# Optimization experiments

Hardware: AMD Instinct MI355X
Metric: run time of the kernel (lower is better)

Reference implementation:

```python
import jax, jax.numpy as jnp
import numpy as np
import math

B, S = 4, 1024
V, D, L, H, F, MAXLEN = 32000, 1024, 6, 16, 4096, 2048
DH = D // H
NUM_BUCKETS, MAX_DIST = 32, 256
REL_SCALE = 64.0 ** 0.5
EPS = 1e-5


def setup_inputs() -> dict:
    key = jax.random.key(0)
    ks = iter(jax.random.split(key, 32))
    sd = 0.02
    inp = {
        'src': jax.random.randint(next(ks), (B, S), 0, V),
        'src_mask': jnp.ones((B, 1, 1, S), dtype=jnp.int32),
        'tok_emb': jax.random.normal(next(ks), (V, D), jnp.float32) * sd,
        'pos_emb': jax.random.normal(next(ks), (MAXLEN, D), jnp.float32) * sd,
        'Wq': jax.random.normal(next(ks), (L, D, D), jnp.float32) * sd,
        'bq': jnp.zeros((L, D), jnp.float32),
        'Wk': jax.random.normal(next(ks), (L, D, D), jnp.float32) * sd,
        'bk': jnp.zeros((L, D), jnp.float32),
        'Wv': jax.random.normal(next(ks), (L, D, D), jnp.float32) * sd,
        'bv': jnp.zeros((L, D), jnp.float32),
        'Wo': jax.random.normal(next(ks), (L, D, D), jnp.float32) * sd,
        'bo': jnp.zeros((L, D), jnp.float32),
        'rel_bias': jax.random.normal(next(ks), (L, NUM_BUCKETS, H), jnp.float32) * sd,
        'ln1_g': jnp.ones((L, D), jnp.float32),
        'ln1_b': jnp.zeros((L, D), jnp.float32),
        'W1': jax.random.normal(next(ks), (L, D, F), jnp.float32) * sd,
        'b1': jnp.zeros((L, F), jnp.float32),
        'W2': jax.random.normal(next(ks), (L, F, D), jnp.float32) * sd,
        'b2': jnp.zeros((L, D), jnp.float32),
        'ln2_g': jnp.ones((L, D), jnp.float32),
        'ln2_b': jnp.zeros((L, D), jnp.float32),
    }
    return inp


def _rel_pos_bucket(seq_len):
    # non-causal bucketing (T5-style), matching the torch source
    q = jnp.arange(seq_len)
    k = jnp.arange(seq_len)
    n = q[:, None] - k[None, :]          # == -(k - q)
    nb = NUM_BUCKETS // 2                # 16
    ret = (n < 0).astype(jnp.int32) * nb
    n = jnp.abs(n)
    max_exact = nb // 2                  # 8
    is_small = n < max_exact
    val_large = max_exact + (
        jnp.log(jnp.maximum(n, 1).astype(jnp.float32) / max_exact)
        / math.log(MAX_DIST / max_exact) * (nb - max_exact)
    ).astype(jnp.int32)
    val_large = jnp.minimum(val_large, nb - 1)
    return ret + jnp.where(is_small, n, val_large)  # [S,S] in [0,32)


def _layer_norm(x, g, b):
    mu = jnp.mean(x, axis=-1, keepdims=True)
    var = jnp.var(x, axis=-1, keepdims=True)
    return (x - mu) * jax.lax.rsqrt(var + EPS) * g + b


def reference(src, src_mask, tok_emb, pos_emb, Wq, bq, Wk, bk, Wv, bv, Wo, bo,
              rel_bias, ln1_g, ln1_b, W1, b1, W2, b2, ln2_g, ln2_b):
    seq_len = src.shape[1]
    bucket = _rel_pos_bucket(seq_len)                      # [S,S] int
    x = tok_emb[src] * jnp.sqrt(jnp.float32(D)) + pos_emb[jnp.arange(seq_len)][None]
    scale = jnp.sqrt(jnp.float32(DH))
    neg = jnp.float32(-1e10)

    def layer(x, p):
        (wq, bq_, wk, bk_, wv, bv_, wo, bo_, rb, g1, b1_, w1, bb1, w2, bb2, g2, b2_) = p
        Q = (x @ wq + bq_).reshape(B, seq_len, H, DH)
        K = (x @ wk + bk_).reshape(B, seq_len, H, DH)
        Vv = (x @ wv + bv_).reshape(B, seq_len, H, DH)
        energy = jnp.einsum('bqhd,bkhd->bhqk', Q, K) / scale
        energy = jnp.where(src_mask == 0, neg, energy)
        bias = rb[bucket]                                  # [S,S,H]
        energy = energy + jnp.transpose(bias, (2, 0, 1))[None] * REL_SCALE
        attn = jax.nn.softmax(energy, axis=-1)
        o = jnp.einsum('bhqk,bkhd->bqhd', attn, Vv).reshape(B, seq_len, D)
        o = o @ wo + bo_
        x = _layer_norm(x + o, g1, b1_)
        f = jax.nn.relu(x @ w1 + bb1) @ w2 + bb2
        x = _layer_norm(x + f, g2, b2_)
        return x, None

    params = (Wq, bq, Wk, bk, Wv, bv, Wo, bo, rel_bias,
              ln1_g, ln1_b, W1, b1, W2, b2, ln2_g, ln2_b)
    x, _ = jax.lax.scan(layer, x, params)
    return x
```

## Files before the change

### kernel.cpp

```cpp
#include <hip/hip_runtime.h>

#define B_ 4
#define S_ 1024
#define D_ 1024
#define F_ 4096
#define H_ 16
#define L_ 6
#define M_ (B_*S_)

typedef unsigned short u16;
typedef __attribute__((ext_vector_type(4))) unsigned short u16x4;
typedef __attribute__((ext_vector_type(8))) short s16x8;
typedef __attribute__((ext_vector_type(8))) __bf16 bf16x8;
typedef __attribute__((ext_vector_type(4))) float f32x4;

typedef const __attribute__((address_space(1))) unsigned int gu32;
typedef __attribute__((address_space(3))) unsigned int su32;

__device__ __forceinline__ u16 f2bf(float f) {
  union { float f; unsigned u; } v; v.f = f;
  unsigned u = v.u;
  return (u16)((u + 0x7fffu + ((u >> 16) & 1u)) >> 16);
}
__device__ __forceinline__ float bf2f(u16 h) {
  union { unsigned u; float f; } v; v.u = (unsigned)h << 16; return v.f;
}

__device__ __forceinline__ f32x4 mfma16(s16x8 a, s16x8 b, f32x4 c) {
  return __builtin_amdgcn_mfma_f32_16x16x32_bf16(
      __builtin_bit_cast(bf16x8, a), __builtin_bit_cast(bf16x8, b), c, 0, 0, 0);
}

__device__ __forceinline__ void gload16(const void* g, void* s) {
  __builtin_amdgcn_global_load_lds((gu32*)g, (su32*)s, 16, 0, 0);
}

template<int OUTMODE>
__device__ __forceinline__ void gemm128_body(
    const u16* __restrict__ A, const u16* __restrict__ Bt,
    const float* __restrict__ b0, const float* __restrict__ b1,
    const float* __restrict__ b2, u16* __restrict__ Ch,
    int N, int K, int kbeg, int kend)
{
  __shared__ __align__(16) u16 As[128 * 64];
  __shared__ __align__(16) u16 Bs[128 * 64];
  const int tid = threadIdx.x, lane = tid & 63, w = tid >> 6;
  const int bm = blockIdx.x * 128, bn = blockIdx.y * 128;
  const int wm = (w >> 1) * 64, wn = (w & 1) * 64;

  f32x4 acc[4][4];
#pragma unroll
  for (int i = 0; i < 4; i++)
#pragma unroll
    for (int j = 0; j < 4; j++) acc[i][j] = {0.f, 0.f, 0.f, 0.f};

  for (int k0 = kbeg; k0 < kend; k0 += 64) {
    __syncthreads();
#pragma unroll
    for (int i = 0; i < 4; i++) {
      const int flat = i * 4096 + w * 1024 + lane * 16;
      const int row = flat >> 7, ce = (flat & 127) >> 1;
      gload16(A + (size_t)(bm + row) * K + k0 + ce, As + i * 2048 + w * 512);
      gload16(Bt + (size_t)(bn + row) * K + k0 + ce, Bs + i * 2048 + w * 512);
    }
    __syncthreads();
#pragma unroll
    for (int kk = 0; kk < 2; kk++) {
      s16x8 af[4], bf[4];
#pragma unroll
      for (int mf = 0; mf < 4; mf++)
        af[mf] = *(const s16x8*)&As[(wm + mf * 16 + (lane & 15)) * 64 + kk * 32 + (lane >> 4) * 8];
#pragma unroll
      for (int nf = 0; nf < 4; nf++)
        bf[nf] = *(const s16x8*)&Bs[(wn + nf * 16 + (lane & 15)) * 64 + kk * 32 + (lane >> 4) * 8];
#pragma unroll
      for (int mf = 0; mf < 4; mf++)
#pragma unroll
        for (int nf = 0; nf < 4; nf++)
          acc[mf][nf] = mfma16(af[mf], bf[nf], acc[mf][nf]);
    }
  }
#pragma unroll
  for (int nf = 0; nf < 4; nf++) {
    const int col = bn + wn + nf * 16 + (lane & 15);
    float bvv = 0.f, sc = 1.0f;
    int zz = 0, lc = col;
    if (OUTMODE == 3) {
      zz = col >> 10; lc = col & 1023;
      const float* bp = (zz == 0) ? b0 : (zz == 1) ? b1 : b2;
      bvv = bp[lc];
      sc = (zz == 0) ? 0.125f : 1.0f;
    }
#pragma unroll
    for (int mf = 0; mf < 4; mf++) {
#pragma unroll
      for (int j = 0; j < 4; j++) {
        const int row = bm + wm + mf * 16 + ((lane >> 4) << 2) + j;
        const float v = acc[mf][nf][j];
        if (OUTMODE == 1) {
          Ch[(size_t)row * N + col] = f2bf(v);
        } else {
          Ch[(size_t)zz * M_ * D_ + (size_t)row * D_ + lc] = f2bf((v + bvv) * sc);
        }
      }
    }
  }
}

__global__ __launch_bounds__(256, 3) void gemm_qkvf(
    const u16* __restrict__ A, const u16* __restrict__ WT,
    const float* __restrict__ bq, const float* __restrict__ bk,
    const float* __restrict__ bv, u16* __restrict__ Out)
{
  gemm128_body<3>(A, WT, bq, bk, bv, Out, 3 * D_, D_, 0, D_);
}

__global__ __launch_bounds__(256, 3) void gemm_osplit2(
    const u16* __restrict__ A, const u16* __restrict__ WT,
    u16* __restrict__ P)
{
  const int z = blockIdx.z;
  gemm128_body<1>(A, WT, nullptr, nullptr, nullptr,
                  P + (size_t)z * M_ * D_, D_, D_, z * 512, z * 512 + 512);
}

__device__ __forceinline__ s16x8 readfrag(const u16* half, int r, int kk, int hi4) {
  const int c = (kk * 64 + hi4 * 16) ^ ((r & 7) << 4);
  return *(const s16x8*)((const char*)half + r * 128 + c);
}

__device__ __forceinline__ void stage_half(
    const u16* __restrict__ src, int ldk, u16* lds_half, int w, int lane)
{
#pragma unroll
  for (int j = 0; j < 2; j++) {
    const int flat = j * 8192 + w * 1024 + lane * 16;
    const int row = flat >> 7;
    const int kb = (flat & 127) ^ ((row & 7) << 4);
    gload16(src + (size_t)row * ldk + (kb >> 1), lds_half + j * 4096 + w * 512);
  }
}

#define BAR     asm volatile("s_barrier" ::: "memory")
#define PH_PRE  asm volatile("s_barrier" ::: "memory"); __builtin_amdgcn_s_setprio(1)
#define PH_POST __builtin_amdgcn_s_setprio(0); __builtin_amdgcn_sched_barrier(0)
#define VM4     asm volatile("s_waitcnt vmcnt(4)" ::: "memory")
#define VM0     asm volatile("s_waitcnt vmcnt(0)" ::: "memory")

#define READ_B(bufhalf) do { \
  _Pragma("unroll") for (int nf = 0; nf < 4; nf++) \
  _Pragma("unroll") for (int kk = 0; kk < 2; kk++) \
    bfr[nf][kk] = readfrag(bufhalf, rb0 + nf * 16 + lo16, kk, hi4); } while (0)
#define READ_A(bufhalf, Q) do { \
  _Pragma("unroll") for (int m = 0; m < 2; m++) \
  _Pragma("unroll") for (int kk = 0; kk < 2; kk++) \
    af[m][kk] = readfrag(bufhalf, (2 * (Q) + m) * 16 + lo16, kk, hi4); } while (0)
#define DO_MFMA(Q) do { \
  _Pragma("unroll") for (int kk = 0; kk < 2; kk++) \
  _Pragma("unroll") for (int m = 0; m < 2; m++) \
  _Pragma("unroll") for (int nf = 0; nf < 4; nf++) \
    acc[2 * (Q) + m][nf] = mfma16(af[m][kk], bfr[nf][kk], acc[2 * (Q) + m][nf]); } while (0)

template<int OUTMODE>
__device__ __forceinline__ void gemm256_body(
    const u16* __restrict__ A, const u16* __restrict__ Bt,
    const float* __restrict__ bias, u16* __restrict__ Ch,
    int N, int K, int kbeg, int kslice)
{
  __shared__ __align__(16) u16 As[2][2][8192];
  __shared__ __align__(16) u16 Bs[2][2][8192];
  const int tid = threadIdx.x, lane = tid & 63, w = tid >> 6;
  const int wr = w >> 2, wc = w & 3;
  const int lo16 = lane & 15, hi4 = lane >> 4;
  const int bm = blockIdx.x * 256, bn = blockIdx.y * 256;
  const int rb0 = (wc & 1) * 64;

  const u16* Abase = A + (size_t)bm * K + kbeg;
  const u16* Bbase = Bt + (size_t)bn * K + kbeg;
  const size_t h1 = (size_t)128 * K;
  const int NT = kslice >> 6, NI = NT >> 1;

  f32x4 acc[8][4];
#pragma unroll
  for (int i = 0; i < 8; i++)
#pragma unroll
    for (int j = 0; j < 4; j++) acc[i][j] = {0.f, 0.f, 0.f, 0.f};

  stage_half(Abase,           K, As[0][0], w, lane);
  stage_half(Abase + h1,      K, As[0][1], w, lane);
  stage_half(Bbase,           K, Bs[0][0], w, lane);
  stage_half(Bbase + h1,      K, Bs[0][1], w, lane);
  stage_half(Abase + 64,      K, As[1][0], w, lane);
  stage_half(Abase + h1 + 64, K, As[1][1], w, lane);
  stage_half(Bbase + 64,      K, Bs[1][0], w, lane);
  stage_half(Bbase + h1 + 64, K, Bs[1][1], w, lane);
  asm volatile("s_waitcnt vmcnt(8)" ::: "memory");
  BAR;

  const u16* Ae = As[0][wr]; const u16* Ao = As[1][wr];
  const u16* Be = Bs[0][wc >> 1]; const u16* Bo = Bs[1][wc >> 1];
  s16x8 af[2][2], bfr[4][2];

  for (int it = 0; it < NI - 1; ++it) {
    READ_B(Be); READ_A(Ae, 0);
    if (it > 0) {
      stage_half(Abase +      (size_t)(2 * it + 1) * 64, K, As[1][0], w, lane);
      stage_half(Abase + h1 + (size_t)(2 * it + 1) * 64, K, As[1][1], w, lane);
    }
    PH_PRE; DO_MFMA(0); PH_POST; BAR;
    READ_A(Ae, 1);
    stage_half(Bbase +      (size_t)(2 * it + 2) * 64, K, Bs[0][0], w, lane);
    PH_PRE; DO_MFMA(1); PH_POST; BAR;
    READ_A(Ae, 2);
    stage_half(Bbase + h1 + (size_t)(2 * it + 2) * 64, K, Bs[0][1], w, lane);
    PH_PRE; DO_MFMA(2); PH_POST; BAR;
    READ_A(Ae, 3);
    PH_PRE; DO_MFMA(3); PH_POST; VM4; BAR;
    READ_B(Bo); READ_A(Ao, 0);
    stage_half(Abase +      (size_t)(2 * it + 2) * 64, K, As[0][0], w, lane);
    stage_half(Abase + h1 + (size_t)(2 * it + 2) * 64, K, As[0][1], w, lane);
    PH_PRE; DO_MFMA(0); PH_POST; BAR;
    READ_A(Ao, 1);
    stage_half(Bbase +      (size_t)(2 * it + 3) * 64, K, Bs[1][0], w, lane);
    PH_PRE; DO_MFMA(1); PH_POST; BAR;
    READ_A(Ao, 2);
    stage_half(Bbase + h1 + (size_t)(2 * it + 3) * 64, K, Bs[1][1], w, lane);
    PH_PRE; DO_MFMA(2); PH_POST; BAR;
    READ_A(Ao, 3);
    PH_PRE; DO_MFMA(3); PH_POST; VM4; BAR;
  }
  READ_B(Be); READ_A(Ae, 0);
  stage_half(Abase +      (size_t)(NT - 1) * 64, K, As[1][0], w, lane);
  stage_half(Abase + h1 + (size_t)(NT - 1) * 64, K, As[1][1], w, lane);
  PH_PRE; DO_MFMA(0); PH_POST; BAR;
  READ_A(Ae, 1);             PH_PRE; DO_MFMA(1); PH_POST; BAR;
  READ_A(Ae, 2);             PH_PRE; DO_MFMA(2); PH_POST; BAR;
  READ_A(Ae, 3);             PH_PRE; DO_MFMA(3); PH_POST; VM0; BAR;
  READ_B(Bo); READ_A(Ao, 0); PH_PRE; DO_MFMA(0); PH_POST; BAR;
  READ_A(Ao, 1);             PH_PRE; DO_MFMA(1); PH_POST; BAR;
  READ_A(Ao, 2);             PH_PRE; DO_MFMA(2); PH_POST; BAR;
  READ_A(Ao, 3);             PH_PRE; DO_MFMA(3); PH_POST;

  const int row0 = bm + wr * 128, col0 = bn + wc * 64;
#pragma unroll
  for (int nf = 0; nf < 4; nf++) {
    const int col = col0 + nf * 16 + lo16;
    const float bv = (OUTMODE == 2) ? bias[col] : 0.f;
#pragma unroll
    for (int mf = 0; mf < 8; mf++) {
#pragma unroll
      for (int j = 0; j < 4; j++) {
        const int row = row0 + mf * 16 + hi4 * 4 + j;
        float v = acc[mf][nf][j];
        if (OUTMODE == 2) v = fmaxf(v + bv, 0.f);
        Ch[(size_t)row * N + col] = f2bf(v);
      }
    }
  }
}

__global__ __launch_bounds__(512, 2) void gemm_ffn1(
    const u16* __restrict__ A, const u16* __restrict__ WT,
    const float* __restrict__ bias, u16* __restrict__ Out)
{
  gemm256_body<2>(A, WT, bias, Out, F_, D_, 0, D_);
}

__global__ __launch_bounds__(512, 2) void gemm_ffn2sp4(
    const u16* __restrict__ A, const u16* __restrict__ WT,
    u16* __restrict__ P)
{
  const int z = blockIdx.z;
  gemm256_body<4>(A, WT, nullptr, P + (size_t)z * M_ * D_,
                  D_, F_, z * 1024, 1024);
}

__global__ __launch_bounds__(256) void transpose_cvt(
    const float* __restrict__ src, u16* __restrict__ dst, int R, int Cc)
{
  __shared__ float t[32][33];
  const int c0 = blockIdx.x * 32, r0 = blockIdx.y * 32;
  const int tx = threadIdx.x & 31, ty = threadIdx.x >> 5;
#pragma unroll
  for (int i = 0; i < 4; i++)
    t[ty + 8 * i][tx] = src[(size_t)(r0 + ty + 8 * i) * Cc + c0 + tx];
  __syncthreads();
#pragma unroll
  for (int i = 0; i < 4; i++)
    dst[(size_t)(c0 + ty + 8 * i) * R + r0 + tx] = f2bf(t[tx][ty + 8 * i]);
}

__global__ __launch_bounds__(256) void transpose4(
    const float* __restrict__ Wq, const float* __restrict__ Wk,
    const float* __restrict__ Wv, const float* __restrict__ Wo,
    u16* __restrict__ WTqkv, u16* __restrict__ WTo)
{
  __shared__ float t[32][33];
  const int z = blockIdx.z;
  const float* src = (z == 0) ? Wq : (z == 1) ? Wk : (z == 2) ? Wv : Wo;
  u16* dst = (z < 3) ? WTqkv + (size_t)z * D_ * D_ : WTo;
  const int c0 = blockIdx.x * 32, r0 = blockIdx.y * 32;
  const int tx = threadIdx.x & 31, ty = threadIdx.x >> 5;
#pragma unroll
  for (int i = 0; i < 4; i++)
    t[ty + 8 * i][tx] = src[(size_t)(r0 + ty + 8 * i) * D_ + c0 + tx];
  __syncthreads();
#pragma unroll
  for (int i = 0; i < 4; i++)
    dst[(size_t)(c0 + ty + 8 * i) * D_ + r0 + tx] = f2bf(t[tx][ty + 8 * i]);
}

__global__ __launch_bounds__(256) void vt_transpose(
    const u16* __restrict__ Vb, u16* __restrict__ Vt)
{
  __shared__ u16 t[64][66];
  const int s0 = blockIdx.x * 64;
  const int bh = blockIdx.y;
  const int b = bh >> 4, h = bh & 15;
  const int tid = threadIdx.x;
  const int row = tid >> 2;
  const int c0 = (tid & 3) * 16;
  const u16* src = Vb + (size_t)(b * S_ + s0 + row) * D_ + h * 64 + c0;
  *(s16x8*)&t[row][c0] = *(const s16x8*)src;
  *(s16x8*)&t[row][c0 + 8] = *(const s16x8*)(src + 8);
  __syncthreads();
  const int dh = tid >> 2;
  const int sc = (tid & 3) * 16;
  s16x8 a, bv;
#pragma unroll
  for (int u = 0; u < 8; u++) a[u] = (short)t[sc + u][dh];
#pragma unroll
  for (int u = 0; u < 8; u++) bv[u] = (short)t[sc + 8 + u][dh];
  u16* dst = Vt + (size_t)(bh * 64 + dh) * S_ + s0 + sc;
  *(s16x8*)dst = a;
  *(s16x8*)(dst + 8) = bv;
}

__global__ __launch_bounds__(256) void build_lut(
    const float* __restrict__ rb, float* __restrict__ lut_g)
{
  const int h = blockIdx.x, l = blockIdx.y;
  for (int idx = threadIdx.x; idx < 2048; idx += 256) {
    const int rel = idx - 1024;
    const int ret = rel < 0 ? 16 : 0;
    const int n = rel < 0 ? -rel : rel;
    int bu;
    if (n < 8) bu = ret + n;
    else {
      const float t = logf((float)n * 0.125f) * (8.0f / 3.4657359027997265f);
      int vl = 8 + (int)t;
      if (vl > 15) vl = 15;
      bu = ret + vl;
    }
    lut_g[(size_t)(l * H_ + h) * 2048 + idx] = rb[l * 512 + bu * 16 + h] * 8.0f;
  }
}

__global__ __launch_bounds__(256) void mask2neg(
    const int* __restrict__ mask, u16* __restrict__ mf)
{
  const int i = blockIdx.x * 256 + threadIdx.x;
  if (i < B_ * S_) mf[i] = mask[i] ? (u16)0 : f2bf(-1e10f);
}

__device__ __forceinline__ s16x8 lds_swz(const u16* base, int row, int cb) {
  const int addr = row * 128 + (cb ^ ((row & 7) << 4));
  return *(const s16x8*)((const char*)base + addr);
}

#define ATTN_STAGE(t, buf) do { \
  const int kt2 = (t) * 64; \
  const int flat2 = tid * 16; \
  const int row2 = flat2 >> 7; \
  const int ce2 = ((flat2 & 127) ^ ((row2 & 7) << 4)) >> 1; \
  gload16(Kb + (size_t)(bS + kt2 + row2) * D_ + hh + ce2, Ks[buf] + w * 512); \
  gload16(Vt + (size_t)(bh * 64 + row2) * S_ + kt2 + ce2, Vs[buf] + w * 512); \
} while (0)

__global__ __launch_bounds__(512, 2) void attn_kernel(
    const u16* __restrict__ Qb, const u16* __restrict__ Kb,
    const u16* __restrict__ Vt, const u16* __restrict__ mask16,
    const float* __restrict__ lut_g, u16* __restrict__ AO)
{
  __shared__ __align__(16) float lut[2048];
  __shared__ __align__(16) u16 maskf[1024];
  __shared__ __align__(16) u16 Ks[2][64 * 64];
  __shared__ __align__(16) u16 Vs[2][64 * 64];
  __shared__ __align__(16) u16 Ps[8][16 * 68];

  const int tid = threadIdx.x;
  const int lane = tid & 63;
  const int w = tid >> 6;
  const int bh = blockIdx.x;
  const int b = bh >> 4, h = bh & 15;
  const int q0 = blockIdx.y * 128 + w * 16;
  const int bS = b * S_, hh = h * 64;
  const int lo16 = lane & 15, hi4 = lane >> 4;

  const float* lsrc = lut_g + (size_t)h * 2048;
  gload16(lsrc + w * 256 + lane * 4, lut + w * 256);
  if (w < 2)
    gload16(mask16 + bS + w * 512 + lane * 8, maskf + w * 512);

  s16x8 qf[2];
#pragma unroll
  for (int kk = 0; kk < 2; kk++)
    qf[kk] = *(const s16x8*)(Qb + (size_t)(bS + q0 + lo16) * D_ + hh +
                             kk * 32 + hi4 * 8);

  s16x8 onesf;
#pragma unroll
  for (int u = 0; u < 8; u++) onesf[u] = (short)((lo16 == 0) ? 0x3F80 : 0);

  f32x4 oacc[5];
#pragma unroll
  for (int i = 0; i < 5; i++) oacc[i] = {0.f, 0.f, 0.f, 0.f};

  ATTN_STAGE(0, 0);
  asm volatile("s_waitcnt vmcnt(0) lgkmcnt(0)" ::: "memory");
  __builtin_amdgcn_s_barrier();

  for (int t = 0; t < S_ / 64; ++t) {
    const int cur = t & 1;
    const int kt = t * 64;
    if (t < S_ / 64 - 1) ATTN_STAGE(t + 1, cur ^ 1);

    f32x4 sacc[4];
#pragma unroll
    for (int i = 0; i < 4; i++) sacc[i] = {0.f, 0.f, 0.f, 0.f};
#pragma unroll
    for (int kk = 0; kk < 2; kk++) {
      const int cb = kk * 64 + hi4 * 16;
#pragma unroll
      for (int nf = 0; nf < 4; nf++) {
        const s16x8 kb = lds_swz(Ks[cur], nf * 16 + lo16, cb);
        sacc[nf] = mfma16(qf[kk], kb, sacc[nf]);
      }
    }

    float kmf[4];
#pragma unroll
    for (int nf = 0; nf < 4; nf++)
      kmf[nf] = bf2f(maskf[kt + nf * 16 + lo16]);

    const int lidx0 = q0 + hi4 * 4 + 1024 - kt - lo16;
#pragma unroll
    for (int j = 0; j < 4; j++) {
      const int lrow = (hi4 << 2) + j;
#pragma unroll
      for (int nf = 0; nf < 4; nf++) {
        const float s = sacc[nf][j] + kmf[nf] + lut[lidx0 + j - nf * 16];
        Ps[w][lrow * 68 + nf * 16 + lo16] = f2bf(__expf(s));
      }
    }

#pragma unroll
    for (int kk = 0; kk < 2; kk++) {
      const s16x8 pa = *(const s16x8*)&Ps[w][lo16 * 68 + kk * 32 + hi4 * 8];
      const int cb = kk * 64 + hi4 * 16;
#pragma unroll
      for (int df = 0; df < 4; df++) {
        const s16x8 vb = lds_swz(Vs[cur], df * 16 + lo16, cb);
        oacc[df] = mfma16(pa, vb, oacc[df]);
      }
      oacc[4] = mfma16(pa, onesf, oacc[4]);
    }

    asm volatile("s_waitcnt vmcnt(0)" ::: "memory");
    __builtin_amdgcn_s_barrier();
  }

  float inv[4];
#pragma unroll
  for (int j = 0; j < 4; j++) {
    const float l = __shfl(oacc[4][j], lane & 48);
    inv[j] = 1.0f / l;
  }
#pragma unroll
  for (int df = 0; df < 4; df++)
#pragma unroll
    for (int j = 0; j < 4; j++) {
      const int qrow = q0 + (hi4 << 2) + j;
      AO[(size_t)(bS + qrow) * D_ + hh + df * 16 + lo16] =
          f2bf(oacc[df][j] * inv[j]);
    }
}

template<int NP>
__global__ __launch_bounds__(256) void ln_fusedb(
    const u16* __restrict__ Xh, const u16* __restrict__ P,
    const float* __restrict__ bias, const float* __restrict__ g,
    const float* __restrict__ be, u16* __restrict__ Yh, float* __restrict__ Yf)
{
  const int row = blockIdx.x;
  const int tid = threadIdx.x;
  const size_t off = (size_t)row * D_;
  const size_t ps = (size_t)M_ * D_;
  const u16x4 xv = ((const u16x4*)(Xh + off))[tid];
  float v[4];
#pragma unroll
  for (int q = 0; q < 4; q++) v[q] = bf2f(xv[q]);
#pragma unroll
  for (int p = 0; p < NP; p++) {
    const u16x4 pv = ((const u16x4*)(P + p * ps + off))[tid];
#pragma unroll
    for (int q = 0; q < 4; q++) v[q] += bf2f(pv[q]);
  }
  const float4 bb = ((const float4*)bias)[tid];
  v[0] += bb.x; v[1] += bb.y; v[2] += bb.z; v[3] += bb.w;

  float sum = v[0] + v[1] + v[2] + v[3];
  float ss = v[0] * v[0] + v[1] * v[1] + v[2] * v[2] + v[3] * v[3];
#pragma unroll
  for (int o = 1; o < 64; o <<= 1) {
    sum += __shfl_xor(sum, o);
    ss += __shfl_xor(ss, o);
  }
  __shared__ float s1[4], s2[4];
  if ((tid & 63) == 0) { s1[tid >> 6] = sum; s2[tid >> 6] = ss; }
  __syncthreads();
  sum = s1[0] + s1[1] + s1[2] + s1[3];
  ss = s2[0] + s2[1] + s2[2] + s2[3];
  const float mu = sum * (1.f / D_);
  const float var = ss * (1.f / D_) - mu * mu;
  const float rstd = rsqrtf(var + 1e-5f);
  const float4 gv = ((const float4*)g)[tid];
  const float4 bv = ((const float4*)be)[tid];
  float y[4];
  y[0] = (v[0] - mu) * rstd * gv.x + bv.x;
  y[1] = (v[1] - mu) * rstd * gv.y + bv.y;
  y[2] = (v[2] - mu) * rstd * gv.z + bv.z;
  y[3] = (v[3] - mu) * rstd * gv.w + bv.w;
  u16x4 hv;
  hv.x = f2bf(y[0]); hv.y = f2bf(y[1]); hv.z = f2bf(y[2]); hv.w = f2bf(y[3]);
  ((u16x4*)(Yh + off))[tid] = hv;
  if (Yf != nullptr) {
    float4 yf; yf.x = y[0]; yf.y = y[1]; yf.z = y[2]; yf.w = y[3];
    ((float4*)(Yf + off))[tid] = yf;
  }
}

__global__ __launch_bounds__(256) void embed_kernel(
    const int* __restrict__ src, const float* __restrict__ tok,
    const float* __restrict__ pos, u16* __restrict__ Xh)
{
  const int row = blockIdx.x;
  const int s = row & (S_ - 1);
  const int t = src[row];
  const int tid = threadIdx.x;
  const float4 tv = ((const float4*)(tok + (size_t)t * D_))[tid];
  const float4 pv = ((const float4*)(pos + (size_t)s * D_))[tid];
  u16x4 hv;
  hv.x = f2bf(tv.x * 32.f + pv.x);
  hv.y = f2bf(tv.y * 32.f + pv.y);
  hv.z = f2bf(tv.z * 32.f + pv.z);
  hv.w = f2bf(tv.w * 32.f + pv.w);
  ((u16x4*)(Xh + (size_t)row * D_))[tid] = hv;
}

extern "C" void kernel_launch(void* const* d_in, const int* in_sizes, int n_in,
                              void* d_out, int out_size, void* d_ws, size_t ws_size,
                              hipStream_t stream)
{
  const int* src = (const int*)d_in[0];
  const int* mask = (const int*)d_in[1];
  const float* tok_emb = (const float*)d_in[2];
  const float* pos_emb = (const float*)d_in[3];
  const float* Wq = (const float*)d_in[4];
  const float* bq = (const float*)d_in[5];
  const float* Wk = (const float*)d_in[6];
  const float* bk = (const float*)d_in[7];
  const float* Wv = (const float*)d_in[8];
  const float* bv = (const float*)d_in[9];
  const float* Wo = (const float*)d_in[10];
  const float* bo = (const float*)d_in[11];
  const float* rb = (const float*)d_in[12];
  const float* g1 = (const float*)d_in[13];
  const float* b1n = (const float*)d_in[14];
  const float* W1 = (const float*)d_in[15];
  const float* b1f = (const float*)d_in[16];
  const float* W2 = (const float*)d_in[17];
  const float* b2f = (const float*)d_in[18];
  const float* g2 = (const float*)d_in[19];
  const float* b2n = (const float*)d_in[20];
  float* out = (float*)d_out;

  char* ws = (char*)d_ws;
  const size_t MB = 1ull << 20;
  u16* xb16  = (u16*)(ws + 0);
  u16* Qb16  = (u16*)(ws + 8 * MB);
  u16* Kb16  = (u16*)(ws + 16 * MB);
  u16* Vb16  = (u16*)(ws + 24 * MB);
  u16* Vt16  = (u16*)(ws + 32 * MB);
  u16* AO16  = (u16*)(ws + 40 * MB);
  u16* Pp16  = (u16*)(ws + 48 * MB);
  u16* WTqkv = (u16*)(ws + 80 * MB);
  u16* WTo   = (u16*)(ws + 86 * MB);
  u16* WT1   = (u16*)(ws + 88 * MB);
  u16* WT2   = (u16*)(ws + 96 * MB);
  u16* Hb16  = (u16*)(ws + 8 * MB);
  float* lut_g  = (float*)(ws + 104 * MB);
  u16*   mask16 = (u16*)(ws + 104 * MB + 786432);

  embed_kernel<<<M_, 256, 0, stream>>>(src, tok_emb, pos_emb, xb16);
  build_lut<<<dim3(H_, L_), 256, 0, stream>>>(rb, lut_g);
  mask2neg<<<(B_ * S_ + 255) / 256, 256, 0, stream>>>(mask, mask16);

  for (int l = 0; l < L_; l++) {
    const size_t oDD = (size_t)l * D_ * D_;
    const size_t oDF = (size_t)l * D_ * F_;

    transpose4<<<dim3(32, 32, 4), 256, 0, stream>>>(
        Wq + oDD, Wk + oDD, Wv + oDD, Wo + oDD, WTqkv, WTo);
    transpose_cvt<<<dim3(F_ / 32, D_ / 32), 256, 0, stream>>>(W1 + oDF, WT1, D_, F_);
    transpose_cvt<<<dim3(D_ / 32, F_ / 32), 256, 0, stream>>>(W2 + oDF, WT2, F_, D_);

    gemm_qkvf<<<dim3(M_ / 128, 3 * D_ / 128), 256, 0, stream>>>(
        xb16, WTqkv, bq + l * D_, bk + l * D_, bv + l * D_, Qb16);

    vt_transpose<<<dim3(S_ / 64, B_ * H_), 256, 0, stream>>>(Vb16, Vt16);

    attn_kernel<<<dim3(B_ * H_, S_ / 128), 512, 0, stream>>>(
        Qb16, Kb16, Vt16, mask16, lut_g + (size_t)l * H_ * 2048, AO16);

    gemm_osplit2<<<dim3(M_ / 128, D_ / 128, 2), 256, 0, stream>>>(
        AO16, WTo, Pp16);

    ln_fusedb<2><<<M_, 256, 0, stream>>>(
        xb16, Pp16, bo + l * D_, g1 + l * D_, b1n + l * D_, xb16, nullptr);

    gemm_ffn1<<<dim3(M_ / 256, F_ / 256), 512, 0, stream>>>(
        xb16, WT1, b1f + l * F_, Hb16);

    gemm_ffn2sp4<<<dim3(M_ / 256, D_ / 256, 4), 512, 0, stream>>>(
        Hb16, WT2, Pp16);

    ln_fusedb<4><<<M_, 256, 0, stream>>>(
        xb16, Pp16, b2f + l * D_, g2 + l * D_, b2n + l * D_, xb16,
        (l == L_ - 1) ? out : nullptr);
  }
}
```

Baseline: 1.282 ms.

## Move QKV and output projections to 256-tile pipelined GEMM; triple-buffer attention K/V

Replaces the simple 128x128 single-buffered GEMM used for the QKV and output projections with the pipelined 256x256 GEMM body already used for the FFN, adding an output mode that scatters Q/K/V with bias and query scaling. Separately, the attention kernel moves from double to triple buffering of K/V tiles, prefetching two tiles ahead and waiting with a partial vmcnt. The intent is higher MFMA utilisation and more load latency hiding. In exchange, the projections run fewer, larger blocks (the output projection gets only 64x2 blocks, which may under-fill the GPU), and attention uses more LDS, which could reduce occupancy.

```diff
diff --git a/kernel.cpp b/kernel.cpp
--- a/kernel.cpp
+++ b/kernel.cpp
@@ -33,95 +33,6 @@
 
 __device__ __forceinline__ void gload16(const void* g, void* s) {
   __builtin_amdgcn_global_load_lds((gu32*)g, (su32*)s, 16, 0, 0);
-}
-
-template<int OUTMODE>
-__device__ __forceinline__ void gemm128_body(
-    const u16* __restrict__ A, const u16* __restrict__ Bt,
-    const float* __restrict__ b0, const float* __restrict__ b1,
-    const float* __restrict__ b2, u16* __restrict__ Ch,
-    int N, int K, int kbeg, int kend)
-{
-  __shared__ __align__(16) u16 As[128 * 64];
-  __shared__ __align__(16) u16 Bs[128 * 64];
-  const int tid = threadIdx.x, lane = tid & 63, w = tid >> 6;
-  const int bm = blockIdx.x * 128, bn = blockIdx.y * 128;
-  const int wm = (w >> 1) * 64, wn = (w & 1) * 64;
-
-  f32x4 acc[4][4];
-#pragma unroll
-  for (int i = 0; i < 4; i++)
-#pragma unroll
-    for (int j = 0; j < 4; j++) acc[i][j] = {0.f, 0.f, 0.f, 0.f};
-
-  for (int k0 = kbeg; k0 < kend; k0 += 64) {
-    __syncthreads();
-#pragma unroll
-    for (int i = 0; i < 4; i++) {
-      const int flat = i * 4096 + w * 1024 + lane * 16;
-      const int row = flat >> 7, ce = (flat & 127) >> 1;
-      gload16(A + (size_t)(bm + row) * K + k0 + ce, As + i * 2048 + w * 512);
-      gload16(Bt + (size_t)(bn + row) * K + k0 + ce, Bs + i * 2048 + w * 512);
-    }
-    __syncthreads();
-#pragma unroll
-    for (int kk = 0; kk < 2; kk++) {
-      s16x8 af[4], bf[4];
-#pragma unroll
-      for (int mf = 0; mf < 4; mf++)
-        af[mf] = *(const s16x8*)&As[(wm + mf * 16 + (lane & 15)) * 64 + kk * 32 + (lane >> 4) * 8];
-#pragma unroll
-      for (int nf = 0; nf < 4; nf++)
-        bf[nf] = *(const s16x8*)&Bs[(wn + nf * 16 + (lane & 15)) * 64 + kk * 32 + (lane >> 4) * 8];
-#pragma unroll
-      for (int mf = 0; mf < 4; mf++)
-#pragma unroll
-        for (int nf = 0; nf < 4; nf++)
-          acc[mf][nf] = mfma16(af[mf], bf[nf], acc[mf][nf]);
-    }
-  }
-#pragma unroll
-  for (int nf = 0; nf < 4; nf++) {
-    const int col = bn + wn + nf * 16 + (lane & 15);
-    float bvv = 0.f, sc = 1.0f;
-    int zz = 0, lc = col;
-    if (OUTMODE == 3) {
-      zz = col >> 10; lc = col & 1023;
-      const float* bp = (zz == 0) ? b0 : (zz == 1) ? b1 : b2;
-      bvv = bp[lc];
-      sc = (zz == 0) ? 0.125f : 1.0f;
-    }
-#pragma unroll
-    for (int mf = 0; mf < 4; mf++) {
-#pragma unroll
-      for (int j = 0; j < 4; j++) {
-        const int row = bm + wm + mf * 16 + ((lane >> 4) << 2) + j;
-        const float v = acc[mf][nf][j];
-        if (OUTMODE == 1) {
-          Ch[(size_t)row * N + col] = f2bf(v);
-        } else {
-          Ch[(size_t)zz * M_ * D_ + (size_t)row * D_ + lc] = f2bf((v + bvv) * sc);
-        }
-      }
-    }
-  }
-}
-
-__global__ __launch_bounds__(256, 3) void gemm_qkvf(
-    const u16* __restrict__ A, const u16* __restrict__ WT,
-    const float* __restrict__ bq, const float* __restrict__ bk,
-    const float* __restrict__ bv, u16* __restrict__ Out)
-{
-  gemm128_body<3>(A, WT, bq, bk, bv, Out, 3 * D_, D_, 0, D_);
-}
-
-__global__ __launch_bounds__(256, 3) void gemm_osplit2(
-    const u16* __restrict__ A, const u16* __restrict__ WT,
-    u16* __restrict__ P)
-{
-  const int z = blockIdx.z;
-  gemm128_body<1>(A, WT, nullptr, nullptr, nullptr,
-                  P + (size_t)z * M_ * D_, D_, D_, z * 512, z * 512 + 512);
 }
 
 __device__ __forceinline__ s16x8 readfrag(const u16* half, int r, int kk, int hi4) {
@@ -164,7 +75,8 @@
 template<int OUTMODE>
 __device__ __forceinline__ void gemm256_body(
     const u16* __restrict__ A, const u16* __restrict__ Bt,
-    const float* __restrict__ bias, u16* __restrict__ Ch,
+    const float* __restrict__ b0, const float* __restrict__ b1,
+    const float* __restrict__ b2, u16* __restrict__ Ch,
     int N, int K, int kbeg, int kslice)
 {
   __shared__ __align__(16) u16 As[2][2][8192];
@@ -241,29 +153,68 @@
   READ_A(Ao, 2);             PH_PRE; DO_MFMA(2); PH_POST; BAR;
   READ_A(Ao, 3);             PH_PRE; DO_MFMA(3); PH_POST;
 
-  const int row0 = bm + wr * 128, col0 = bn + wc * 64;
-#pragma unroll
-  for (int nf = 0; nf < 4; nf++) {
-    const int col = col0 + nf * 16 + lo16;
-    const float bv = (OUTMODE == 2) ? bias[col] : 0.f;
-#pragma unroll
-    for (int mf = 0; mf < 8; mf++) {
-#pragma unroll
-      for (int j = 0; j < 4; j++) {
-        const int row = row0 + mf * 16 + hi4 * 4 + j;
-        float v = acc[mf][nf][j];
-        if (OUTMODE == 2) v = fmaxf(v + bv, 0.f);
-        Ch[(size_t)row * N + col] = f2bf(v);
+  const int row0 = bm + wr * 128;
+  if (OUTMODE == 5) {
+    const int z = bn >> 10;
+    const int lcb = (bn & 1023) + wc * 64;
+    const float* bp = (z == 0) ? b0 : (z == 1) ? b1 : b2;
+    const float sc = (z == 0) ? 0.125f : 1.0f;
+    u16* Outz = Ch + (size_t)z * M_ * D_;
+#pragma unroll
+    for (int nf = 0; nf < 4; nf++) {
+      const int col = lcb + nf * 16 + lo16;
+      const float bv = bp[col];
+#pragma unroll
+      for (int mf = 0; mf < 8; mf++) {
+#pragma unroll
+        for (int j = 0; j < 4; j++) {
+          const int row = row0 + mf * 16 + hi4 * 4 + j;
+          Outz[(size_t)row * D_ + col] = f2bf((acc[mf][nf][j] + bv) * sc);
+        }
       }
     }
-  }
+  } else {
+    const int col0 = bn + wc * 64;
+#pragma unroll
+    for (int nf = 0; nf < 4; nf++) {
+      const int col = col0 + nf * 16 + lo16;
+      const float bv = (OUTMODE == 2) ? b0[col] : 0.f;
+#pragma unroll
+      for (int mf = 0; mf < 8; mf++) {
+#pragma unroll
+        for (int j = 0; j < 4; j++) {
+          const int row = row0 + mf * 16 + hi4 * 4 + j;
+          float v = acc[mf][nf][j];
+          if (OUTMODE == 2) v = fmaxf(v + bv, 0.f);
+          Ch[(size_t)row * N + col] = f2bf(v);
+        }
+      }
+    }
+  }
+}
+
+__global__ __launch_bounds__(512, 2) void gemm_qkvf256(
+    const u16* __restrict__ A, const u16* __restrict__ WT,
+    const float* __restrict__ bq, const float* __restrict__ bk,
+    const float* __restrict__ bv, u16* __restrict__ Out)
+{
+  gemm256_body<5>(A, WT, bq, bk, bv, Out, 3 * D_, D_, 0, D_);
+}
+
+__global__ __launch_bounds__(512, 2) void gemm_osp2_256(
+    const u16* __restrict__ A, const u16* __restrict__ WT,
+    u16* __restrict__ P)
+{
+  const int z = blockIdx.z;
+  gemm256_body<4>(A, WT, nullptr, nullptr, nullptr,
+                  P + (size_t)z * M_ * D_, D_, D_, z * 512, 512);
 }
 
 __global__ __launch_bounds__(512, 2) void gemm_ffn1(
     const u16* __restrict__ A, const u16* __restrict__ WT,
     const float* __restrict__ bias, u16* __restrict__ Out)
 {
-  gemm256_body<2>(A, WT, bias, Out, F_, D_, 0, D_);
+  gemm256_body<2>(A, WT, bias, nullptr, nullptr, Out, F_, D_, 0, D_);
 }
 
 __global__ __launch_bounds__(512, 2) void gemm_ffn2sp4(
@@ -271,8 +222,8 @@
     u16* __restrict__ P)
 {
   const int z = blockIdx.z;
-  gemm256_body<4>(A, WT, nullptr, P + (size_t)z * M_ * D_,
-                  D_, F_, z * 1024, 1024);
+  gemm256_body<4>(A, WT, nullptr, nullptr, nullptr,
+                  P + (size_t)z * M_ * D_, D_, F_, z * 1024, 1024);
 }
 
 __global__ __launch_bounds__(256) void transpose_cvt(
@@ -384,8 +335,8 @@
 {
   __shared__ __align__(16) float lut[2048];
   __shared__ __align__(16) u16 maskf[1024];
-  __shared__ __align__(16) u16 Ks[2][64 * 64];
-  __shared__ __align__(16) u16 Vs[2][64 * 64];
+  __shared__ __align__(16) u16 Ks[3][64 * 64];
+  __shared__ __align__(16) u16 Vs[3][64 * 64];
   __shared__ __align__(16) u16 Ps[8][16 * 68];
 
   const int tid = threadIdx.x;
@@ -417,13 +368,15 @@
   for (int i = 0; i < 5; i++) oacc[i] = {0.f, 0.f, 0.f, 0.f};
 
   ATTN_STAGE(0, 0);
-  asm volatile("s_waitcnt vmcnt(0) lgkmcnt(0)" ::: "memory");
-  __builtin_amdgcn_s_barrier();
+  ATTN_STAGE(1, 1);
 
   for (int t = 0; t < S_ / 64; ++t) {
-    const int cur = t & 1;
+    const int bc = t % 3;
     const int kt = t * 64;
-    if (t < S_ / 64 - 1) ATTN_STAGE(t + 1, cur ^ 1);
+
+    asm volatile("s_waitcnt vmcnt(2)" ::: "memory");
+    __builtin_amdgcn_s_barrier();
+    if (t + 2 < S_ / 64) ATTN_STAGE(t + 2, (t + 2) % 3);
 
     f32x4 sacc[4];
 #pragma unroll
@@ -433,7 +386,7 @@
       const int cb = kk * 64 + hi4 * 16;
 #pragma unroll
       for (int nf = 0; nf < 4; nf++) {
-        const s16x8 kb = lds_swz(Ks[cur], nf * 16 + lo16, cb);
+        const s16x8 kb = lds_swz(Ks[bc], nf * 16 + lo16, cb);
         sacc[nf] = mfma16(qf[kk], kb, sacc[nf]);
       }
     }
@@ -460,14 +413,11 @@
       const int cb = kk * 64 + hi4 * 16;
 #pragma unroll
       for (int df = 0; df < 4; df++) {
-        const s16x8 vb = lds_swz(Vs[cur], df * 16 + lo16, cb);
+        const s16x8 vb = lds_swz(Vs[bc], df * 16 + lo16, cb);
         oacc[df] = mfma16(pa, vb, oacc[df]);
       }
       oacc[4] = mfma16(pa, onesf, oacc[4]);
     }
-
-    asm volatile("s_waitcnt vmcnt(0)" ::: "memory");
-    __builtin_amdgcn_s_barrier();
   }
 
   float inv[4];
@@ -615,7 +565,7 @@
     transpose_cvt<<<dim3(F_ / 32, D_ / 32), 256, 0, stream>>>(W1 + oDF, WT1, D_, F_);
     transpose_cvt<<<dim3(D_ / 32, F_ / 32), 256, 0, stream>>>(W2 + oDF, WT2, F_, D_);
 
-    gemm_qkvf<<<dim3(M_ / 128, 3 * D_ / 128), 256, 0, stream>>>(
+    gemm_qkvf256<<<dim3(M_ / 256, 3 * D_ / 256), 512, 0, stream>>>(
         xb16, WTqkv, bq + l * D_, bk + l * D_, bv + l * D_, Qb16);
 
     vt_transpose<<<dim3(S_ / 64, B_ * H_), 256, 0, stream>>>(Vb16, Vt16);
@@ -623,7 +573,7 @@
     attn_kernel<<<dim3(B_ * H_, S_ / 128), 512, 0, stream>>>(
         Qb16, Kb16, Vt16, mask16, lut_g + (size_t)l * H_ * 2048, AO16);
 
-    gemm_osplit2<<<dim3(M_ / 128, D_ / 128, 2), 256, 0, stream>>>(
+    gemm_osp2_256<<<dim3(M_ / 256, D_ / 256, 2), 512, 0, stream>>>(
         AO16, WTo, Pp16);
 
     ln_fusedb<2><<<M_, 256, 0, stream>>>(
```

After: 1.352 ms. +5.5%, slower.
